# Performance work log

Hardware: AMD Instinct MI355X
Metric: run time of the kernel (lower is better)

The kernel has to match this reference:

```python
import jax, jax.numpy as jnp
import numpy as np

# Module config (from init_kwargs): causal=False, window_size=(256,256), window_type=0,
# softmax_scale=None -> 1/sqrt(D), dropout=0 (eval mode).
WINDOW_LEFT, WINDOW_RIGHT = 256, 256


def _window_mask(Sq, Sk, causal, use_window_mask):
    """Boolean [Sq, Sk] visibility mask, FA2 semantics (right-aligned offset)."""
    qi = jnp.arange(Sq)[:, None]
    kj = jnp.arange(Sk)[None, :]
    offset = Sk - Sq
    if causal:
        return kj <= qi + offset  # window (-1, 0)
    if use_window_mask:
        m = jnp.ones((Sq, Sk), dtype=bool)
        if WINDOW_LEFT >= 0:
            m = m & (kj >= qi + offset - WINDOW_LEFT)
        if WINDOW_RIGHT >= 0:
            m = m & (kj <= qi + offset + WINDOW_RIGHT)
        return m
    return None  # full attention


def setup_inputs() -> dict:
    key = jax.random.key(0)
    kq, kkv = jax.random.split(key)
    B, Sq, Sk, H, D = 2, 2048, 2048, 16, 64
    q = jax.random.normal(kq, (B, Sq, H, D), dtype=jnp.float32)
    kv = jax.random.normal(kkv, (B, Sk, 2, H, D), dtype=jnp.float32)
    return {"q": q, "kv": kv, "causal": 0, "use_window_mask": 1, "return_attn_probs": 0}


def reference(q, kv, causal, use_window_mask, return_attn_probs):
    # q: (B, Sq, H, D); kv: (B, Sk, 2, H, D)
    B, Sq, H, D = q.shape
    Sk = kv.shape[1]
    k = kv[:, :, 0]  # (B, Sk, H, D)
    v = kv[:, :, 1]
    scale = 1.0 / (D ** 0.5)
    scores = jnp.einsum('bqhd,bkhd->bhqk', q, k) * scale  # (B, H, Sq, Sk)
    mask = _window_mask(Sq, Sk, bool(causal), bool(use_window_mask))
    if mask is not None:
        scores = jnp.where(mask[None, None], scores, jnp.finfo(scores.dtype).min)
    probs = jax.nn.softmax(scores, axis=-1)
    out = jnp.einsum('bhqk,bkhd->bqhd', probs, v)  # (B, Sq, H, D)
    return out
```

## Files before the change

### kernel.cpp

```cpp
#include <hip/hip_runtime.h>
#include <hip/hip_bf16.h>

#define B_    2
#define SQ_   2048
#define SK_   2048
#define NH_   16
#define DH_   64
#define WIN_  256
#define NEG_  -30000.0f

typedef __bf16 bf16_t;
typedef bf16_t bf16x8 __attribute__((ext_vector_type(8)));
typedef bf16_t bf16x4 __attribute__((ext_vector_type(4)));
typedef float  f32x4  __attribute__((ext_vector_type(4)));

#define KSTRIDE 72
#define VSTRIDE 72
#define PSTRIDE 72

__global__ __launch_bounds__(512, 4)
void fa_fwd(const float* __restrict__ qg, const float* __restrict__ kvg,
            float* __restrict__ outg) {
  const int tid  = threadIdx.x;
  const int wid  = tid >> 6;
  const int lane = tid & 63;
  const int quad = lane >> 4;
  const int li   = lane & 15;

  const int bid = blockIdx.x;
  const int qb  = bid >> 5;
  const int bh  = bid & 31;
  const int b   = bh >> 4;
  const int h   = bh & 15;

  const int q0b = qb * 128;
  const int q0  = q0b + wid * 16;

  __shared__ __align__(16) bf16_t sK [2][64 * KSTRIDE];
  __shared__ __align__(16) bf16_t sVT[2][64 * VSTRIDE];
  __shared__ __align__(16) bf16_t sP [8][16 * PSTRIDE];
  bf16_t* pl = sP[wid];

  const float qscale = 0.125f * 1.44269504088896340736f;
  const float* qrow = qg + ((size_t)((b * SQ_ + q0 + li) * NH_ + h)) * DH_;
  bf16x8 qfrag[2];
#pragma unroll
  for (int c = 0; c < 2; ++c) {
    f32x4 a0 = *(const f32x4*)(qrow + c * 32 + quad * 8);
    f32x4 a1 = *(const f32x4*)(qrow + c * 32 + quad * 8 + 4);
#pragma unroll
    for (int i = 0; i < 4; ++i) {
      qfrag[c][i]     = (bf16_t)(a0[i] * qscale);
      qfrag[c][i + 4] = (bf16_t)(a1[i] * qscale);
    }
  }

  f32x4 oacc[4];
#pragma unroll
  for (int t = 0; t < 4; ++t) { f32x4 z = {0.f, 0.f, 0.f, 0.f}; oacc[t] = z; }
  float m = NEG_, l = 0.f;

  int klo = q0b - WIN_; if (klo < 0) klo = 0;
  int khi = q0b + 127 + WIN_ + 1; if (khi > SK_) khi = SK_;

  const float* kbase = kvg + (size_t)b * SK_ * 2 * NH_ * DH_ + (size_t)h * DH_;
  const float* vbase = kbase + NH_ * DH_;
  const size_t krow_stride = 2 * NH_ * DH_;

  const int skey = tid >> 3;
  const int sd0  = (tid & 7) * 8;
  const int vcol = skey ^ (((sd0 >> 3) & 7) << 3);

  f32x4 ka[2], va[2];
  {
    const float* kr = kbase + (size_t)(klo + skey) * krow_stride + sd0;
    const float* vr = vbase + (size_t)(klo + skey) * krow_stride + sd0;
    ka[0] = *(const f32x4*)kr;       ka[1] = *(const f32x4*)(kr + 4);
    va[0] = *(const f32x4*)vr;       va[1] = *(const f32x4*)(vr + 4);
  }
  {
    bf16x8 w;
#pragma unroll
    for (int i = 0; i < 4; ++i) { w[i] = (bf16_t)ka[0][i]; w[i + 4] = (bf16_t)ka[1][i]; }
    *(bf16x8*)(&sK[0][skey * KSTRIDE + sd0]) = w;
#pragma unroll
    for (int i = 0; i < 4; ++i) {
      sVT[0][(sd0 + i)     * VSTRIDE + vcol] = (bf16_t)va[0][i];
      sVT[0][(sd0 + 4 + i) * VSTRIDE + vcol] = (bf16_t)va[1][i];
    }
  }
  __syncthreads();

  int buf = 0;
  for (int kk = klo; kk < khi; kk += 64) {
    const bool nxt = (kk + 64 < khi);
    if (nxt) {
      const float* kr = kbase + (size_t)(kk + 64 + skey) * krow_stride + sd0;
      const float* vr = vbase + (size_t)(kk + 64 + skey) * krow_stride + sd0;
      ka[0] = *(const f32x4*)kr;       ka[1] = *(const f32x4*)(kr + 4);
      va[0] = *(const f32x4*)vr;       va[1] = *(const f32x4*)(vr + 4);
    }

    if (kk + 63 >= q0 - WIN_ && kk <= q0 + 15 + WIN_) {
      f32x4 sc[4];
#pragma unroll
      for (int s = 0; s < 4; ++s) {
        bf16x8 kf0 = *(const bf16x8*)(&sK[buf][(s * 16 + li) * KSTRIDE + quad * 8]);
        bf16x8 kf1 = *(const bf16x8*)(&sK[buf][(s * 16 + li) * KSTRIDE + 32 + quad * 8]);
        f32x4 acc = {0.f, 0.f, 0.f, 0.f};
        acc = __builtin_amdgcn_mfma_f32_16x16x32_bf16(kf0, qfrag[0], acc, 0, 0, 0);
        acc = __builtin_amdgcn_mfma_f32_16x16x32_bf16(kf1, qfrag[1], acc, 0, 0, 0);
        sc[s] = acc;
      }
      if (kk < q0 - 241 || kk > q0 + 193) {
        const int qa = q0 + li;
#pragma unroll
        for (int s = 0; s < 4; ++s)
#pragma unroll
          for (int r = 0; r < 4; ++r) {
            int key = kk + s * 16 + quad * 4 + r;
            unsigned dd = (unsigned)(key - qa + WIN_);
            if (dd > 2u * WIN_) sc[s][r] = NEG_;
          }
      }
      float tmax = NEG_;
#pragma unroll
      for (int s = 0; s < 4; ++s)
        tmax = fmaxf(tmax, fmaxf(fmaxf(sc[s][0], sc[s][1]), fmaxf(sc[s][2], sc[s][3])));
      tmax = fmaxf(tmax, __shfl_xor(tmax, 16));
      tmax = fmaxf(tmax, __shfl_xor(tmax, 32));
      float mnew  = fmaxf(m, tmax);
      float alpha = exp2f(m - mnew);
      float psum = 0.f;
#pragma unroll
      for (int s = 0; s < 4; ++s) {
        bf16x4 pk;
#pragma unroll
        for (int r = 0; r < 4; ++r) {
          float p = exp2f(sc[s][r] - mnew);
          psum += p;
          pk[r] = (bf16_t)p;
        }
        *(bf16x4*)(&pl[li * PSTRIDE + s * 16 + quad * 4]) = pk;
      }
      psum += __shfl_xor(psum, 16);
      psum += __shfl_xor(psum, 32);
      l = l * alpha + psum;
      m = mnew;

      asm volatile("s_waitcnt lgkmcnt(0)" ::: "memory");

      float al[4];
#pragma unroll
      for (int r = 0; r < 4; ++r) al[r] = __shfl(alpha, quad * 4 + r);
#pragma unroll
      for (int t = 0; t < 4; ++t) {
        oacc[t][0] *= al[0]; oacc[t][1] *= al[1];
        oacc[t][2] *= al[2]; oacc[t][3] *= al[3];
      }
#pragma unroll
      for (int kc = 0; kc < 2; ++kc) {
        bf16x8 pf = *(const bf16x8*)(&pl[li * PSTRIDE + kc * 32 + quad * 8]);
#pragma unroll
        for (int t = 0; t < 4; ++t) {
          const int d = 16 * t + li;
          const int c = ((2 * t + (li >> 3)) & 7) << 3;
          bf16x8 vf = *(const bf16x8*)(&sVT[buf][d * VSTRIDE + ((kc * 32 + quad * 8) ^ c)]);
          oacc[t] = __builtin_amdgcn_mfma_f32_16x16x32_bf16(pf, vf, oacc[t], 0, 0, 0);
        }
      }
    }

    if (nxt) {
      bf16x8 w;
#pragma unroll
      for (int i = 0; i < 4; ++i) { w[i] = (bf16_t)ka[0][i]; w[i + 4] = (bf16_t)ka[1][i]; }
      *(bf16x8*)(&sK[buf ^ 1][skey * KSTRIDE + sd0]) = w;
#pragma unroll
      for (int i = 0; i < 4; ++i) {
        sVT[buf ^ 1][(sd0 + i)     * VSTRIDE + vcol] = (bf16_t)va[0][i];
        sVT[buf ^ 1][(sd0 + 4 + i) * VSTRIDE + vcol] = (bf16_t)va[1][i];
      }
    }
    __syncthreads();
    buf ^= 1;
  }

  float rl[4];
#pragma unroll
  for (int r = 0; r < 4; ++r) {
    float lv = __shfl(l, quad * 4 + r);
    rl[r] = 1.0f / lv;
  }
  float* orow = outg + ((size_t)((b * SQ_ + q0) * NH_ + h)) * DH_;
#pragma unroll
  for (int t = 0; t < 4; ++t)
#pragma unroll
    for (int r = 0; r < 4; ++r)
      orow[(size_t)(quad * 4 + r) * (NH_ * DH_) + 16 * t + li] = oacc[t][r] * rl[r];
}

extern "C" void kernel_launch(void* const* d_in, const int* in_sizes, int n_in,
                              void* d_out, int out_size, void* d_ws, size_t ws_size,
                              hipStream_t stream) {
  (void)in_sizes; (void)n_in; (void)out_size; (void)d_ws; (void)ws_size;
  const float* q  = (const float*)d_in[0];
  const float* kv = (const float*)d_in[1];
  float* out = (float*)d_out;
  dim3 grid(B_ * NH_ * (SQ_ / 128));
  fa_fwd<<<grid, 512, 0, stream>>>(q, kv, out);
}
```

Before: 111.9 us.

## Use 128-key tiles, keep P in registers, skip out-of-window MFMA subtiles

Doubles the key tile to 128 so there are half as many barriers and loop iterations. Each tile is processed as two 64-key halves. The P matrix now goes straight from the softmax registers into the PV MFMA, with a key permutation matched to the V layout, which removes the per-wave LDS round trip and the lgkmcnt wait. V is loaded as columns per wave and written transposed into LDS with vector stores. QK and PV MFMAs for 16- and 32-key subtiles entirely outside the window are skipped. The costs are more registers for prefetch (16 scalar V loads per thread) and more LDS, which may limit occupancy under the 4-block launch bound.

Result: slower. 156.9 us (+40.2%).

```diff
diff --git a/kernel.cpp b/kernel.cpp
--- a/kernel.cpp
+++ b/kernel.cpp
@@ -8,6 +8,7 @@
 #define DH_   64
 #define WIN_  256
 #define NEG_  -30000.0f
+#define TK    128
 
 typedef __bf16 bf16_t;
 typedef bf16_t bf16x8 __attribute__((ext_vector_type(8)));
@@ -15,8 +16,7 @@
 typedef float  f32x4  __attribute__((ext_vector_type(4)));
 
 #define KSTRIDE 72
-#define VSTRIDE 72
-#define PSTRIDE 72
+#define VSTRIDE 136
 
 __global__ __launch_bounds__(512, 4)
 void fa_fwd(const float* __restrict__ qg, const float* __restrict__ kvg,
@@ -36,10 +36,8 @@
   const int q0b = qb * 128;
   const int q0  = q0b + wid * 16;
 
-  __shared__ __align__(16) bf16_t sK [2][64 * KSTRIDE];
+  __shared__ __align__(16) bf16_t sK [2][TK * KSTRIDE];
   __shared__ __align__(16) bf16_t sVT[2][64 * VSTRIDE];
-  __shared__ __align__(16) bf16_t sP [8][16 * PSTRIDE];
-  bf16_t* pl = sP[wid];
 
   const float qscale = 0.125f * 1.44269504088896340736f;
   const float* qrow = qg + ((size_t)((b * SQ_ + q0 + li) * NH_ + h)) * DH_;
@@ -65,123 +63,132 @@
 
   const float* kbase = kvg + (size_t)b * SK_ * 2 * NH_ * DH_ + (size_t)h * DH_;
   const float* vbase = kbase + NH_ * DH_;
-  const size_t krow_stride = 2 * NH_ * DH_;
-
-  const int skey = tid >> 3;
-  const int sd0  = (tid & 7) * 8;
-  const int vcol = skey ^ (((sd0 >> 3) & 7) << 3);
-
-  f32x4 ka[2], va[2];
-  {
-    const float* kr = kbase + (size_t)(klo + skey) * krow_stride + sd0;
-    const float* vr = vbase + (size_t)(klo + skey) * krow_stride + sd0;
-    ka[0] = *(const f32x4*)kr;       ka[1] = *(const f32x4*)(kr + 4);
-    va[0] = *(const f32x4*)vr;       va[1] = *(const f32x4*)(vr + 4);
-  }
-  {
-    bf16x8 w;
-#pragma unroll
-    for (int i = 0; i < 4; ++i) { w[i] = (bf16_t)ka[0][i]; w[i + 4] = (bf16_t)ka[1][i]; }
-    *(bf16x8*)(&sK[0][skey * KSTRIDE + sd0]) = w;
+  const size_t krow = 2 * NH_ * DH_;
+
+  const int skey = tid >> 2;
+  const int sd0  = (tid & 3) * 16;
+  const int vg   = (lane >> 3) & 7;
+
+  f32x4 ka[4]; float vv[16];
+
+  auto load_tile = [&](int kt) {
+    const float* kr = kbase + (size_t)(kt + skey) * krow + sd0;
+#pragma unroll
+    for (int i = 0; i < 4; ++i) ka[i] = *(const f32x4*)(kr + 4 * i);
+    const float* vr = vbase + (size_t)(kt + wid * 16) * krow + lane;
+#pragma unroll
+    for (int j = 0; j < 16; ++j) vv[j] = vr[(size_t)j * krow];
+  };
+  auto stage = [&](int bw) {
+    bf16x8 u0, u1;
 #pragma unroll
     for (int i = 0; i < 4; ++i) {
-      sVT[0][(sd0 + i)     * VSTRIDE + vcol] = (bf16_t)va[0][i];
-      sVT[0][(sd0 + 4 + i) * VSTRIDE + vcol] = (bf16_t)va[1][i];
+      u0[i] = (bf16_t)ka[0][i]; u0[i + 4] = (bf16_t)ka[1][i];
+      u1[i] = (bf16_t)ka[2][i]; u1[i + 4] = (bf16_t)ka[3][i];
     }
-  }
+    *(bf16x8*)&sK[bw][skey * KSTRIDE + sd0]     = u0;
+    *(bf16x8*)&sK[bw][skey * KSTRIDE + sd0 + 8] = u1;
+    bf16x8 w0, w1;
+#pragma unroll
+    for (int j = 0; j < 8; ++j) { w0[j] = (bf16_t)vv[j]; w1[j] = (bf16_t)vv[8 + j]; }
+    *(bf16x8*)&sVT[bw][lane * VSTRIDE + (((2 * wid)     ^ vg) << 3)] = w0;
+    *(bf16x8*)&sVT[bw][lane * VSTRIDE + (((2 * wid + 1) ^ vg) << 3)] = w1;
+  };
+
+  load_tile(klo);
+  stage(0);
   __syncthreads();
 
+  const int wlo = q0 - WIN_;
+  const int whi = q0 + 15 + WIN_;
+
   int buf = 0;
-  for (int kk = klo; kk < khi; kk += 64) {
-    const bool nxt = (kk + 64 < khi);
-    if (nxt) {
-      const float* kr = kbase + (size_t)(kk + 64 + skey) * krow_stride + sd0;
-      const float* vr = vbase + (size_t)(kk + 64 + skey) * krow_stride + sd0;
-      ka[0] = *(const f32x4*)kr;       ka[1] = *(const f32x4*)(kr + 4);
-      va[0] = *(const f32x4*)vr;       va[1] = *(const f32x4*)(vr + 4);
-    }
-
-    if (kk + 63 >= q0 - WIN_ && kk <= q0 + 15 + WIN_) {
-      f32x4 sc[4];
-#pragma unroll
-      for (int s = 0; s < 4; ++s) {
-        bf16x8 kf0 = *(const bf16x8*)(&sK[buf][(s * 16 + li) * KSTRIDE + quad * 8]);
-        bf16x8 kf1 = *(const bf16x8*)(&sK[buf][(s * 16 + li) * KSTRIDE + 32 + quad * 8]);
-        f32x4 acc = {0.f, 0.f, 0.f, 0.f};
-        acc = __builtin_amdgcn_mfma_f32_16x16x32_bf16(kf0, qfrag[0], acc, 0, 0, 0);
-        acc = __builtin_amdgcn_mfma_f32_16x16x32_bf16(kf1, qfrag[1], acc, 0, 0, 0);
-        sc[s] = acc;
-      }
-      if (kk < q0 - 241 || kk > q0 + 193) {
-        const int qa = q0 + li;
+  for (int kk = klo; kk < khi; kk += TK) {
+    const bool nxt = (kk + TK < khi);
+    if (nxt) load_tile(kk + TK);
+
+#pragma unroll
+    for (int hf = 0; hf < 2; ++hf) {
+      const int kb = kk + hf * 64;
+      if (kb + 63 >= wlo && kb <= whi) {
+        f32x4 sc[4];
+#pragma unroll
+        for (int s = 0; s < 4; ++s) {
+          const int k0 = kb + s * 16;
+          if (k0 + 15 >= wlo && k0 <= whi) {
+            const int row = (hf * 64 + s * 16 + li) * KSTRIDE;
+            bf16x8 kf0 = *(const bf16x8*)&sK[buf][row + quad * 8];
+            bf16x8 kf1 = *(const bf16x8*)&sK[buf][row + 32 + quad * 8];
+            f32x4 acc = {0.f, 0.f, 0.f, 0.f};
+            acc = __builtin_amdgcn_mfma_f32_16x16x32_bf16(kf0, qfrag[0], acc, 0, 0, 0);
+            acc = __builtin_amdgcn_mfma_f32_16x16x32_bf16(kf1, qfrag[1], acc, 0, 0, 0);
+            sc[s] = acc;
+          } else {
+            f32x4 z = {NEG_, NEG_, NEG_, NEG_}; sc[s] = z;
+          }
+        }
+        if (kb < q0 - 241 || kb > q0 + 193) {
+          const int qa = q0 + li;
+#pragma unroll
+          for (int s = 0; s < 4; ++s)
+#pragma unroll
+            for (int r = 0; r < 4; ++r) {
+              int key = kb + s * 16 + quad * 4 + r;
+              unsigned dd = (unsigned)(key - qa + WIN_);
+              if (dd > 2u * WIN_) sc[s][r] = NEG_;
+            }
+        }
+        float tmax = NEG_;
 #pragma unroll
         for (int s = 0; s < 4; ++s)
+          tmax = fmaxf(tmax, fmaxf(fmaxf(sc[s][0], sc[s][1]), fmaxf(sc[s][2], sc[s][3])));
+        tmax = fmaxf(tmax, __shfl_xor(tmax, 16));
+        tmax = fmaxf(tmax, __shfl_xor(tmax, 32));
+        float mnew  = fmaxf(m, tmax);
+        float alpha = exp2f(m - mnew);
+        float psum = 0.f;
+        bf16x8 pa[2];
+#pragma unroll
+        for (int s = 0; s < 4; ++s)
 #pragma unroll
           for (int r = 0; r < 4; ++r) {
-            int key = kk + s * 16 + quad * 4 + r;
-            unsigned dd = (unsigned)(key - qa + WIN_);
-            if (dd > 2u * WIN_) sc[s][r] = NEG_;
+            float p = exp2f(sc[s][r] - mnew);
+            psum += p;
+            pa[s >> 1][(s & 1) * 4 + r] = (bf16_t)p;
           }
-      }
-      float tmax = NEG_;
-#pragma unroll
-      for (int s = 0; s < 4; ++s)
-        tmax = fmaxf(tmax, fmaxf(fmaxf(sc[s][0], sc[s][1]), fmaxf(sc[s][2], sc[s][3])));
-      tmax = fmaxf(tmax, __shfl_xor(tmax, 16));
-      tmax = fmaxf(tmax, __shfl_xor(tmax, 32));
-      float mnew  = fmaxf(m, tmax);
-      float alpha = exp2f(m - mnew);
-      float psum = 0.f;
-#pragma unroll
-      for (int s = 0; s < 4; ++s) {
-        bf16x4 pk;
-#pragma unroll
-        for (int r = 0; r < 4; ++r) {
-          float p = exp2f(sc[s][r] - mnew);
-          psum += p;
-          pk[r] = (bf16_t)p;
-        }
-        *(bf16x4*)(&pl[li * PSTRIDE + s * 16 + quad * 4]) = pk;
-      }
-      psum += __shfl_xor(psum, 16);
-      psum += __shfl_xor(psum, 32);
-      l = l * alpha + psum;
-      m = mnew;
-
-      asm volatile("s_waitcnt lgkmcnt(0)" ::: "memory");
-
-      float al[4];
-#pragma unroll
-      for (int r = 0; r < 4; ++r) al[r] = __shfl(alpha, quad * 4 + r);
-#pragma unroll
-      for (int t = 0; t < 4; ++t) {
-        oacc[t][0] *= al[0]; oacc[t][1] *= al[1];
-        oacc[t][2] *= al[2]; oacc[t][3] *= al[3];
-      }
-#pragma unroll
-      for (int kc = 0; kc < 2; ++kc) {
-        bf16x8 pf = *(const bf16x8*)(&pl[li * PSTRIDE + kc * 32 + quad * 8]);
+        psum += __shfl_xor(psum, 16);
+        psum += __shfl_xor(psum, 32);
+        l = l * alpha + psum;
+        m = mnew;
+        float al[4];
+#pragma unroll
+        for (int r = 0; r < 4; ++r) al[r] = __shfl(alpha, quad * 4 + r);
 #pragma unroll
         for (int t = 0; t < 4; ++t) {
-          const int d = 16 * t + li;
-          const int c = ((2 * t + (li >> 3)) & 7) << 3;
-          bf16x8 vf = *(const bf16x8*)(&sVT[buf][d * VSTRIDE + ((kc * 32 + quad * 8) ^ c)]);
-          oacc[t] = __builtin_amdgcn_mfma_f32_16x16x32_bf16(pf, vf, oacc[t], 0, 0, 0);
+          oacc[t][0] *= al[0]; oacc[t][1] *= al[1];
+          oacc[t][2] *= al[2]; oacc[t][3] *= al[3];
+        }
+#pragma unroll
+        for (int kc = 0; kc < 2; ++kc) {
+          const int c0 = kb + kc * 32;
+          if (c0 + 31 >= wlo && c0 <= whi) {
+            const int c8lo = hf * 8 + 4 * kc + (quad >> 1);
+#pragma unroll
+            for (int t = 0; t < 4; ++t) {
+              const int d = 16 * t + li;
+              const int g = (d >> 3) & 7;
+              const int rowo = d * VSTRIDE + (quad & 1) * 4;
+              bf16x4 lo = *(const bf16x4*)&sVT[buf][rowo + ((c8lo       ^ g) << 3)];
+              bf16x4 hi = *(const bf16x4*)&sVT[buf][rowo + (((c8lo + 2) ^ g) << 3)];
+              bf16x8 vf = {lo[0], lo[1], lo[2], lo[3], hi[0], hi[1], hi[2], hi[3]};
+              oacc[t] = __builtin_amdgcn_mfma_f32_16x16x32_bf16(pa[kc], vf, oacc[t], 0, 0, 0);
+            }
+          }
         }
       }
     }
 
-    if (nxt) {
-      bf16x8 w;
-#pragma unroll
-      for (int i = 0; i < 4; ++i) { w[i] = (bf16_t)ka[0][i]; w[i + 4] = (bf16_t)ka[1][i]; }
-      *(bf16x8*)(&sK[buf ^ 1][skey * KSTRIDE + sd0]) = w;
-#pragma unroll
-      for (int i = 0; i < 4; ++i) {
-        sVT[buf ^ 1][(sd0 + i)     * VSTRIDE + vcol] = (bf16_t)va[0][i];
-        sVT[buf ^ 1][(sd0 + 4 + i) * VSTRIDE + vcol] = (bf16_t)va[1][i];
-      }
-    }
+    if (nxt) stage(buf ^ 1);
     __syncthreads();
     buf ^= 1;
   }
```
